# Performance work log

Measured on AMD Instinct MI355X. Metric: run time of the kernel, lower is better.

The kernel has to match this reference:

```python
import jax, jax.numpy as jnp
import numpy as np

NUM_CLUSTERS = 16
CHANNELS = 256
UPDATE_RATE = 0.2
# channels % num_clusters == 0 -> all cluster capacities equal
_BASE = CHANNELS // NUM_CLUSTERS
_REM = CHANNELS % NUM_CLUSTERS
CLUSTER_SIZES = jnp.asarray([_BASE + 1] * _REM + [_BASE] * (NUM_CLUSTERS - _REM), dtype=jnp.int32)


def _cdist(a, b):
    # euclidean pairwise distance, batched over leading dims
    d2 = (jnp.sum(a * a, -1)[..., :, None]
          + jnp.sum(b * b, -1)[..., None, :]
          - 2.0 * (a @ jnp.swapaxes(b, -1, -2)))
    return jnp.sqrt(jnp.clip(d2, 0.0))


def _fps(D, k):
    # farthest point sampling given full [N,N] distance matrix
    start = jnp.argmax(D.sum(1))
    def step(min_d, _):
        far = jnp.argmax(min_d)
        return jnp.minimum(min_d, D[far]), far
    _, rest = jax.lax.scan(step, D[start], None, length=k - 1)
    return jnp.concatenate([start[None], rest])


def _capacity_assign(D, sizes):
    # greedy fixed-capacity assignment, sequential over channels
    order = jnp.argsort(D, axis=1)  # [C, K] cluster preference per channel
    def step(counts, row):
        avail = counts[row] < sizes[row]
        chosen = row[jnp.argmax(avail)]  # first available preference
        return counts.at[chosen].add(1), chosen
    _, assign = jax.lax.scan(step, jnp.zeros(sizes.shape[0], jnp.int32), order)
    return assign


def setup_inputs() -> dict:
    key = jax.random.key(0)
    k1, k2 = jax.random.split(key)
    features = jax.random.normal(k1, (8, CHANNELS, 64, 256), dtype=jnp.float32)
    pos_emb_batch = jax.random.normal(k2, (8, CHANNELS, 3), dtype=jnp.float32)
    return {"features": features, "pos_emb_batch": pos_emb_batch}


def reference(features, pos_emb_batch):
    b, c, nw, df = features.shape
    K = NUM_CLUSTERS
    pos = pos_emb_batch[0]                                   # [C, 3] (module's pos_emb buffer)
    # _initialize_centers: FPS over electrode positions
    centers = pos[_fps(_cdist(pos, pos), K)]                 # [K, 3]
    # _find_farthest_channels (euclidean): FPS over flattened features per batch
    ff = features.reshape(b, c, -1)
    Db = _cdist(ff, ff)                                      # [b, C, C]
    sel = jax.vmap(lambda D: _fps(D, K))(Db)                 # [b, K]
    # _cluster_euclidean_temp: nearest temp center per channel
    center_coords = pos_emb_batch[jnp.arange(b)[:, None], sel]      # [b, K, 3]
    temp_assign = jnp.argmin(_cdist(pos_emb_batch, center_coords), -1)  # [b, C]
    # per-cluster mean of positions over the whole batch
    flat_a = temp_assign.reshape(-1)
    flat_p = pos_emb_batch.reshape(-1, 3)
    sums = jax.ops.segment_sum(flat_p, flat_a, num_segments=K)
    cnts = jax.ops.segment_sum(jnp.ones(flat_a.shape, jnp.float32), flat_a, num_segments=K)
    avg = jnp.where(cnts[:, None] > 0, sums / jnp.maximum(cnts, 1.0)[:, None], 0.0)
    # match old centers to batch-average temp centers and EMA update
    matching = jnp.argmin(_cdist(centers, avg), axis=1)
    centers = (1.0 - UPDATE_RATE) * centers + UPDATE_RATE * avg[matching]
    # capacity-constrained final assignment
    return _capacity_assign(_cdist(pos, centers), CLUSTER_SIZES)
```

## Files before the change

kernel.cpp:

```cpp
#include <hip/hip_runtime.h>

#define NB 8
#define NC 256
#define DF 16384
#define KCL 16
#define SPLITS 16
#define KC (DF / SPLITS)
#define BK 32
#define ITERS (KC / BK)
#define NPAIR 3
#define GEMM_BLOCKS (NPAIR * 2 * NB * SPLITS)

typedef _Float16 half8 __attribute__((ext_vector_type(8)));
typedef _Float16 half4_t __attribute__((ext_vector_type(4)));
typedef float floatx4 __attribute__((ext_vector_type(4)));

__device__ const int TItab[NPAIR] = {0,0,1};
__device__ const int TJtab[NPAIR] = {0,1,1};

__device__ __forceinline__ int argmax256w(float v, float* sv, int* si) {
  int t = threadIdx.x;
  float bv = v; int bi = t;
  #pragma unroll
  for (int s = 32; s >= 1; s >>= 1) {
    float ov = __shfl_down(bv, s);
    int   oi = __shfl_down(bi, s);
    if (ov > bv || (ov == bv && oi < bi)) { bv = ov; bi = oi; }
  }
  int w = t >> 6;
  if ((t & 63) == 0) { sv[w] = bv; si[w] = bi; }
  __syncthreads();
  float rbv = sv[0]; int rbi = si[0];
  #pragma unroll
  for (int k = 1; k < 4; ++k) {
    float ov = sv[k]; int oi = si[k];
    if (ov > rbv || (ov == rbv && oi < rbi)) { rbv = ov; rbi = oi; }
  }
  __syncthreads();
  return rbi;
}

__device__ __forceinline__ int argmax512p(float v, float* sv, int* si) {
  int t = threadIdx.x;
  sv[t] = v; si[t] = t;
  __syncthreads();
  #pragma unroll
  for (int s = 256; s >= 1; s >>= 1) {
    if (t < s) {
      float a = sv[t], b = sv[t + s];
      int ia = si[t], ib = si[t + s];
      if (b > a || (b == a && ib < ia)) { sv[t] = b; si[t] = ib; }
    }
    __syncthreads();
  }
  int r = si[0];
  __syncthreads();
  return r;
}

__global__ __launch_bounds__(512, 6) void k_gemm_pre(const float* __restrict__ ff,
                                                     const float* __restrict__ pe,
                                                     float* __restrict__ Pp,
                                                     float* __restrict__ centers0,
                                                     float* __restrict__ rs,
                                                     float* __restrict__ dgp) {
  __shared__ _Float16 Ah[128][40];
  __shared__ _Float16 Al[128][40];
  __shared__ _Float16 Bh[64][40];
  __shared__ _Float16 Bl[64][40];

  const int bid = blockIdx.x;
  const int tid = threadIdx.x;

  if (bid == GEMM_BLOCKS) {
    float* sm = (float*)&Ah[0][0];
    float* px = sm;        float* py = sm + 256;
    float* pz = sm + 512;  float* pn = sm + 768;
    float* sv = sm + 1024; int*   si = (int*)(sm + 1536);
    int* fpsIdx = (int*)(sm + 2048);
    const int t = tid;
    for (int i = t; i < NB * NC; i += 512) rs[i] = 0.f;
    const bool valid = t < NC;
    float x = 0.f, y = 0.f, z = 0.f, n = 0.f;
    if (valid) {
      x = pe[t * 3 + 0]; y = pe[t * 3 + 1]; z = pe[t * 3 + 2];
      n = x * x + y * y + z * z;
      px[t] = x; py[t] = y; pz[t] = z; pn[t] = n;
    }
    __syncthreads();
    float rsum = -3.4e38f;
    if (valid) {
      rsum = 0.f;
      for (int j = 0; j < NC; ++j) {
        float dot = x * px[j] + y * py[j] + z * pz[j];
        rsum += sqrtf(fmaxf(n + pn[j] - 2.f * dot, 0.f));
      }
    }
    int start = argmax512p(rsum, sv, si);
    if (t == 0) fpsIdx[0] = start;
    float mind = -3.4e38f;
    if (valid) {
      float dot0 = x * px[start] + y * py[start] + z * pz[start];
      mind = sqrtf(fmaxf(n + pn[start] - 2.f * dot0, 0.f));
    }
    for (int it = 1; it < KCL; ++it) {
      int far = argmax512p(mind, sv, si);
      if (t == 0) fpsIdx[it] = far;
      if (valid) {
        float dot = x * px[far] + y * py[far] + z * pz[far];
        mind = fminf(mind, sqrtf(fmaxf(n + pn[far] - 2.f * dot, 0.f)));
      }
    }
    __syncthreads();
    if (t < KCL) {
      int p = fpsIdx[t];
      centers0[t * 3 + 0] = px[p];
      centers0[t * 3 + 1] = py[p];
      centers0[t * 3 + 2] = pz[p];
    }
    return;
  }

  const int x    = bid & 7;
  const int slot = bid >> 3;
  const int tc   = slot % 6;
  const int u    = slot / 6;
  const int gi   = x * 16 + u;
  const int b    = gi & 7;
  const int sp   = gi >> 3;

  const int pair = tc >> 1, ch = tc & 1;
  const int ti = TItab[pair], tj = TJtab[pair];
  const bool diag = (ti == tj);

  const int wave = tid >> 6, lane = tid & 63;
  const int wr = wave >> 1, wc = wave & 1;
  const int lrow = lane & 15, q = lane >> 4;

  const int srA = tid >> 2, scA = (tid & 3) * 8;
  const int srB = tid >> 3, scB = (tid & 7) * 4;
  const float* gA = ff + ((size_t)(b * NC + ti * 128 + srA)) * DF + sp * KC + scA;
  const float* gB = ff + ((size_t)(b * NC + tj * 128 + ch * 64 + srB)) * DF + sp * KC + scB;

  floatx4 a1[2][2], c23[2][2];
  #pragma unroll
  for (int i = 0; i < 2; ++i)
    #pragma unroll
    for (int j = 0; j < 2; ++j) { a1[i][j] = (floatx4)0.f; c23[i][j] = (floatx4)0.f; }

  float4 ra0 = *(const float4*)(gA), ra1 = *(const float4*)(gA + 4);
  float4 rb = make_float4(0.f, 0.f, 0.f, 0.f);
  if (!diag) rb = *(const float4*)(gB);
  gA += BK; gB += BK;

  for (int it = 0; it < ITERS; ++it) {
    float fa[8] = {ra0.x, ra0.y, ra0.z, ra0.w, ra1.x, ra1.y, ra1.z, ra1.w};
    half8 ah, al;
    #pragma unroll
    for (int e = 0; e < 8; ++e) {
      _Float16 h = (_Float16)fa[e];
      ah[e] = h;
      al[e] = (_Float16)(fa[e] - (float)h);
    }
    half4_t bh4 = (half4_t)(_Float16)0.f, bl4 = (half4_t)(_Float16)0.f;
    if (!diag) {
      float fb[4] = {rb.x, rb.y, rb.z, rb.w};
      #pragma unroll
      for (int e = 0; e < 4; ++e) {
        _Float16 h = (_Float16)fb[e];
        bh4[e] = h;
        bl4[e] = (_Float16)(fb[e] - (float)h);
      }
    }
    __syncthreads();
    *(half8*)&Ah[srA][scA] = ah;
    *(half8*)&Al[srA][scA] = al;
    if (!diag) {
      *(half4_t*)&Bh[srB][scB] = bh4;
      *(half4_t*)&Bl[srB][scB] = bl4;
    }
    __syncthreads();
    if (it + 1 < ITERS) {
      ra0 = *(const float4*)(gA); ra1 = *(const float4*)(gA + 4);
      if (!diag) rb = *(const float4*)(gB);
      gA += BK; gB += BK;
    }
    const _Float16* bhp = diag ? &Ah[ch * 64][0] : &Bh[0][0];
    const _Float16* blp = diag ? &Al[ch * 64][0] : &Bl[0][0];
    half8 af[2], lf[2];
    #pragma unroll
    for (int i = 0; i < 2; ++i) {
      af[i] = *(const half8*)&Ah[wr * 32 + i * 16 + lrow][q * 8];
      lf[i] = *(const half8*)&Al[wr * 32 + i * 16 + lrow][q * 8];
    }
    #pragma unroll
    for (int j = 0; j < 2; ++j) {
      half8 bhf = *(const half8*)(bhp + (wc * 32 + j * 16 + lrow) * 40 + q * 8);
      half8 blf = *(const half8*)(blp + (wc * 32 + j * 16 + lrow) * 40 + q * 8);
      #pragma unroll
      for (int i = 0; i < 2; ++i) {
        a1[i][j]  = __builtin_amdgcn_mfma_f32_16x16x32_f16(af[i], bhf, a1[i][j], 0, 0, 0);
        c23[i][j] = __builtin_amdgcn_mfma_f32_16x16x32_f16(af[i], blf, c23[i][j], 0, 0, 0);
        c23[i][j] = __builtin_amdgcn_mfma_f32_16x16x32_f16(lf[i], bhf, c23[i][j], 0, 0, 0);
      }
    }
  }

  float* Pb = Pp + (size_t)(sp * NB + b) * NC * NC;
  #pragma unroll
  for (int i = 0; i < 2; ++i) {
    int grow = ti * 128 + wr * 32 + i * 16 + q * 4;
    #pragma unroll
    for (int j = 0; j < 2; ++j) {
      int gcol = tj * 128 + ch * 64 + wc * 32 + j * 16 + lrow;
      float4 v;
      v.x = a1[i][j][0] + c23[i][j][0];
      v.y = a1[i][j][1] + c23[i][j][1];
      v.z = a1[i][j][2] + c23[i][j][2];
      v.w = a1[i][j][3] + c23[i][j][3];
      Pb[(size_t)(grow + 0) * NC + gcol] = v.x;
      Pb[(size_t)(grow + 1) * NC + gcol] = v.y;
      Pb[(size_t)(grow + 2) * NC + gcol] = v.z;
      Pb[(size_t)(grow + 3) * NC + gcol] = v.w;
      if (!diag) {
        *(float4*)&Pb[(size_t)gcol * NC + grow] = v;
      } else {
        int dr = gcol - grow;
        if (dr >= 0 && dr < 4) {
          float vr = (dr == 0) ? v.x : (dr == 1) ? v.y : (dr == 2) ? v.z : v.w;
          dgp[(sp * NB + b) * NC + gcol] = vr;
        }
      }
    }
  }
}

__global__ __launch_bounds__(256) void k_formD(const float* __restrict__ Pp,
                                               const float* __restrict__ dgp,
                                               float* __restrict__ Db,
                                               float* __restrict__ rs,
                                               int* __restrict__ fps_done) {
  const int t = threadIdx.x;
  const int b = blockIdx.x >> 8;
  const int i = blockIdx.x & 255;
  if (blockIdx.x == 0 && t == 0) *fps_done = 0;
  float dgt = 0.f;
  #pragma unroll
  for (int sp = 0; sp < SPLITS; ++sp)
    dgt += dgp[(sp * NB + b) * NC + t];
  __shared__ float dgi_s;
  if (t == i) dgi_s = dgt;
  __syncthreads();
  float dgi = dgi_s;
  float acc = 0.f;
  #pragma unroll
  for (int sp = 0; sp < SPLITS; ++sp)
    acc += Pp[((size_t)(sp * NB + b) * NC + i) * NC + t];
  float d2 = dgi + dgt - 2.f * acc;
  float d = sqrtf(fmaxf(d2, 0.f));
  Db[((size_t)b * NC + i) * NC + t] = d;
  atomicAdd(&rs[b * NC + t], d);
}

__global__ __launch_bounds__(256) void k_fps_final(const float* __restrict__ Db,
                                                   const float* __restrict__ rs,
                                                   const float* __restrict__ pe,
                                                   const float* __restrict__ centers0,
                                                   float* __restrict__ ccoord,
                                                   int* __restrict__ fps_done,
                                                   int* __restrict__ outp) {
  const int b = blockIdx.x, t = threadIdx.x;
  __shared__ float sv[4]; __shared__ int si[4];
  __shared__ int fpsIdx[KCL];
  {
    const float* D = Db + (size_t)b * NC * NC;
    int start = argmax256w(rs[b * NC + t], sv, si);
    if (t == 0) fpsIdx[0] = start;
    float mind = D[start * NC + t];
    for (int it = 1; it < KCL; ++it) {
      int far = argmax256w(mind, sv, si);
      if (t == 0) fpsIdx[it] = far;
      mind = fminf(mind, D[far * NC + t]);
    }
    __syncthreads();
    if (t < KCL) {
      int p = fpsIdx[t];
      ccoord[(b * KCL + t) * 3 + 0] = pe[(b * NC + p) * 3 + 0];
      ccoord[(b * KCL + t) * 3 + 1] = pe[(b * NC + p) * 3 + 1];
      ccoord[(b * KCL + t) * 3 + 2] = pe[(b * NC + p) * 3 + 2];
    }
  }
  __syncthreads();
  if (t == 0)
    __hip_atomic_fetch_add(fps_done, 1, __ATOMIC_RELEASE, __HIP_MEMORY_SCOPE_AGENT);
  if (b != 0) return;

  if (t == 0) {
    while (__hip_atomic_load(fps_done, __ATOMIC_ACQUIRE, __HIP_MEMORY_SCOPE_AGENT) < NB)
      __builtin_amdgcn_s_sleep(8);
  }
  __syncthreads();

  __shared__ float cc[NB * KCL * 3];
  __shared__ float cn[NB * KCL];
  __shared__ float sums[KCL][3];
  __shared__ int cnts[KCL];
  __shared__ float avg[KCL][3];
  __shared__ float an[KCL];
  __shared__ float c0[KCL * 3];
  __shared__ float c1x[KCL], c1y[KCL], c1z[KCL], c1n[KCL];
  __shared__ int order[NC][KCL];
  for (int i = t; i < NB * KCL * 3; i += 256) cc[i] = ccoord[i];
  if (t < KCL * 3) c0[t] = centers0[t];
  if (t < KCL) { sums[t][0] = 0.f; sums[t][1] = 0.f; sums[t][2] = 0.f; cnts[t] = 0; }
  __syncthreads();
  if (t < NB * KCL) {
    float x = cc[t * 3], y = cc[t * 3 + 1], z = cc[t * 3 + 2];
    cn[t] = x * x + y * y + z * z;
  }
  __syncthreads();
  for (int bb = 0; bb < NB; ++bb) {
    int p = bb * NC + t;
    float x = pe[p * 3], y = pe[p * 3 + 1], z = pe[p * 3 + 2];
    float n = x * x + y * y + z * z;
    float best = 3.4e38f; int bi = 0;
    #pragma unroll
    for (int k = 0; k < KCL; ++k) {
      int c = bb * KCL + k;
      float dot = x * cc[c * 3] + y * cc[c * 3 + 1] + z * cc[c * 3 + 2];
      float d2 = fmaxf(n + cn[c] - 2.f * dot, 0.f);
      if (d2 < best) { best = d2; bi = k; }
    }
    atomicAdd(&sums[bi][0], x);
    atomicAdd(&sums[bi][1], y);
    atomicAdd(&sums[bi][2], z);
    atomicAdd(&cnts[bi], 1);
  }
  __syncthreads();
  if (t < KCL) {
    float c = (float)cnts[t];
    float inv = 1.f / fmaxf(c, 1.f);
    float ax = (cnts[t] > 0) ? sums[t][0] * inv : 0.f;
    float ay = (cnts[t] > 0) ? sums[t][1] * inv : 0.f;
    float az = (cnts[t] > 0) ? sums[t][2] * inv : 0.f;
    avg[t][0] = ax; avg[t][1] = ay; avg[t][2] = az;
    an[t] = ax * ax + ay * ay + az * az;
  }
  __syncthreads();
  if (t < KCL) {
    float x = c0[t * 3], y = c0[t * 3 + 1], z = c0[t * 3 + 2];
    float n = x * x + y * y + z * z;
    float best = 3.4e38f; int bi = 0;
    #pragma unroll
    for (int j = 0; j < KCL; ++j) {
      float dot = x * avg[j][0] + y * avg[j][1] + z * avg[j][2];
      float d2 = fmaxf(n + an[j] - 2.f * dot, 0.f);
      if (d2 < best) { best = d2; bi = j; }
    }
    float nx = 0.8f * x + 0.2f * avg[bi][0];
    float ny = 0.8f * y + 0.2f * avg[bi][1];
    float nz = 0.8f * z + 0.2f * avg[bi][2];
    c1x[t] = nx; c1y[t] = ny; c1z[t] = nz;
    c1n[t] = nx * nx + ny * ny + nz * nz;
  }
  __syncthreads();
  {
    float x = pe[t * 3], y = pe[t * 3 + 1], z = pe[t * 3 + 2];
    float n = x * x + y * y + z * z;
    float v[KCL];
    #pragma unroll
    for (int k = 0; k < KCL; ++k) {
      float dot = x * c1x[k] + y * c1y[k] + z * c1z[k];
      v[k] = fmaxf(n + c1n[k] - 2.f * dot, 0.f);
    }
    bool used[KCL];
    #pragma unroll
    for (int k = 0; k < KCL; ++k) used[k] = false;
    for (int r = 0; r < KCL; ++r) {
      float best = 3.4e38f; int bi = 0;
      #pragma unroll
      for (int j = 0; j < KCL; ++j) {
        if (!used[j] && v[j] < best) { best = v[j]; bi = j; }
      }
      order[t][r] = bi;
      used[bi] = true;
    }
  }
  __syncthreads();
  if (t < 64) {
    int cnt = 0;
    int cur = (t < KCL) ? order[0][t] : 0;
    for (int i = 0; i < NC; ++i) {
      int nxt = (t < KCL && i + 1 < NC) ? order[i + 1][t] : 0;
      int ccur = __shfl(cnt, cur);
      bool avail = (t < KCL) && (ccur < 16);
      unsigned long long m = __ballot(avail);
      int chosen;
      if (m != 0ull) {
        int rank = __ffsll((unsigned long long)m) - 1;
        chosen = __shfl(cur, rank);
      } else {
        chosen = __shfl(cur, 0);
      }
      if (t == chosen) cnt++;
      if (t == 0) outp[i] = chosen;
      cur = nxt;
    }
  }
}

extern "C" void kernel_launch(void* const* d_in, const int* in_sizes, int n_in,
                              void* d_out, int out_size, void* d_ws, size_t ws_size,
                              hipStream_t stream) {
  (void)in_sizes; (void)n_in; (void)out_size; (void)ws_size;
  const float* features = (const float*)d_in[0];
  const float* pe = (const float*)d_in[1];
  char* ws = (char*)d_ws;
  float* Pp       = (float*)(ws);
  float* Db       = (float*)(ws + 33554432);
  float* rs       = (float*)(ws + 35651584);
  float* centers0 = (float*)(ws + 35659776);
  float* ccoord   = (float*)(ws + 35660288);
  float* dgp      = (float*)(ws + 35661824);
  int*   fps_done = (int*)  (ws + 35678208);
  int*   outp     = (int*)d_out;

  hipLaunchKernelGGL(k_gemm_pre, dim3(GEMM_BLOCKS + 1), dim3(512), 0, stream,
                     features, pe, Pp, centers0, rs, dgp);
  hipLaunchKernelGGL(k_formD, dim3(2048), dim3(256), 0, stream,
                     Pp, dgp, Db, rs, fps_done);
  hipLaunchKernelGGL(k_fps_final, dim3(NB), dim3(256), 0, stream,
                     Db, rs, pe, centers0, ccoord, fps_done, outp);
}
```

Before: 339.8 us.

## Double-buffer LDS tiles in split-fp16 Gram GEMM to drop a barrier per iteration

The shared-memory A/B hi/lo tiles become double-buffered, so each iteration converts and stores the next K-slice into the alternate buffer while MFMAs consume the current one. This leaves one __syncthreads per iteration instead of two. The MFMA section is also wrapped in s_setprio raises. LDS use doubles and the occupancy hint drops from 6 to 4 blocks per CU, which could reduce latency hiding for the global loads.

```diff
diff --git a/kernel.cpp b/kernel.cpp
--- a/kernel.cpp
+++ b/kernel.cpp
@@ -58,22 +58,22 @@
   return r;
 }
 
-__global__ __launch_bounds__(512, 6) void k_gemm_pre(const float* __restrict__ ff,
+__global__ __launch_bounds__(512, 4) void k_gemm_pre(const float* __restrict__ ff,
                                                      const float* __restrict__ pe,
                                                      float* __restrict__ Pp,
                                                      float* __restrict__ centers0,
                                                      float* __restrict__ rs,
                                                      float* __restrict__ dgp) {
-  __shared__ _Float16 Ah[128][40];
-  __shared__ _Float16 Al[128][40];
-  __shared__ _Float16 Bh[64][40];
-  __shared__ _Float16 Bl[64][40];
+  __shared__ _Float16 Ah[2][128][40];
+  __shared__ _Float16 Al[2][128][40];
+  __shared__ _Float16 Bh[2][64][40];
+  __shared__ _Float16 Bl[2][64][40];
 
   const int bid = blockIdx.x;
   const int tid = threadIdx.x;
 
   if (bid == GEMM_BLOCKS) {
-    float* sm = (float*)&Ah[0][0];
+    float* sm = (float*)&Ah[0][0][0];
     float* px = sm;        float* py = sm + 256;
     float* pz = sm + 512;  float* pn = sm + 768;
     float* sv = sm + 1024; int*   si = (int*)(sm + 1536);
@@ -152,47 +152,71 @@
   float4 rb = make_float4(0.f, 0.f, 0.f, 0.f);
   if (!diag) rb = *(const float4*)(gB);
   gA += BK; gB += BK;
-
-  for (int it = 0; it < ITERS; ++it) {
+  {
     float fa[8] = {ra0.x, ra0.y, ra0.z, ra0.w, ra1.x, ra1.y, ra1.z, ra1.w};
     half8 ah, al;
     #pragma unroll
     for (int e = 0; e < 8; ++e) {
       _Float16 h = (_Float16)fa[e];
-      ah[e] = h;
-      al[e] = (_Float16)(fa[e] - (float)h);
-    }
-    half4_t bh4 = (half4_t)(_Float16)0.f, bl4 = (half4_t)(_Float16)0.f;
+      ah[e] = h; al[e] = (_Float16)(fa[e] - (float)h);
+    }
+    *(half8*)&Ah[0][srA][scA] = ah;
+    *(half8*)&Al[0][srA][scA] = al;
     if (!diag) {
       float fb[4] = {rb.x, rb.y, rb.z, rb.w};
+      half4_t bh4, bl4;
       #pragma unroll
       for (int e = 0; e < 4; ++e) {
         _Float16 h = (_Float16)fb[e];
-        bh4[e] = h;
-        bl4[e] = (_Float16)(fb[e] - (float)h);
-      }
-    }
-    __syncthreads();
-    *(half8*)&Ah[srA][scA] = ah;
-    *(half8*)&Al[srA][scA] = al;
-    if (!diag) {
-      *(half4_t*)&Bh[srB][scB] = bh4;
-      *(half4_t*)&Bl[srB][scB] = bl4;
-    }
-    __syncthreads();
+        bh4[e] = h; bl4[e] = (_Float16)(fb[e] - (float)h);
+      }
+      *(half4_t*)&Bh[0][srB][scB] = bh4;
+      *(half4_t*)&Bl[0][srB][scB] = bl4;
+    }
+  }
+  ra0 = *(const float4*)(gA); ra1 = *(const float4*)(gA + 4);
+  if (!diag) rb = *(const float4*)(gB);
+  gA += BK; gB += BK;
+  __syncthreads();
+
+  for (int it = 0; it < ITERS; ++it) {
+    const int cur = it & 1;
     if (it + 1 < ITERS) {
-      ra0 = *(const float4*)(gA); ra1 = *(const float4*)(gA + 4);
-      if (!diag) rb = *(const float4*)(gB);
-      gA += BK; gB += BK;
-    }
-    const _Float16* bhp = diag ? &Ah[ch * 64][0] : &Bh[0][0];
-    const _Float16* blp = diag ? &Al[ch * 64][0] : &Bl[0][0];
+      float fa[8] = {ra0.x, ra0.y, ra0.z, ra0.w, ra1.x, ra1.y, ra1.z, ra1.w};
+      half8 ah, al;
+      #pragma unroll
+      for (int e = 0; e < 8; ++e) {
+        _Float16 h = (_Float16)fa[e];
+        ah[e] = h; al[e] = (_Float16)(fa[e] - (float)h);
+      }
+      *(half8*)&Ah[cur ^ 1][srA][scA] = ah;
+      *(half8*)&Al[cur ^ 1][srA][scA] = al;
+      if (!diag) {
+        float fb[4] = {rb.x, rb.y, rb.z, rb.w};
+        half4_t bh4, bl4;
+        #pragma unroll
+        for (int e = 0; e < 4; ++e) {
+          _Float16 h = (_Float16)fb[e];
+          bh4[e] = h; bl4[e] = (_Float16)(fb[e] - (float)h);
+        }
+        *(half4_t*)&Bh[cur ^ 1][srB][scB] = bh4;
+        *(half4_t*)&Bl[cur ^ 1][srB][scB] = bl4;
+      }
+      if (it + 2 < ITERS) {
+        ra0 = *(const float4*)(gA); ra1 = *(const float4*)(gA + 4);
+        if (!diag) rb = *(const float4*)(gB);
+        gA += BK; gB += BK;
+      }
+    }
+    const _Float16* bhp = diag ? &Ah[cur][ch * 64][0] : &Bh[cur][0][0];
+    const _Float16* blp = diag ? &Al[cur][ch * 64][0] : &Bl[cur][0][0];
     half8 af[2], lf[2];
     #pragma unroll
     for (int i = 0; i < 2; ++i) {
-      af[i] = *(const half8*)&Ah[wr * 32 + i * 16 + lrow][q * 8];
-      lf[i] = *(const half8*)&Al[wr * 32 + i * 16 + lrow][q * 8];
-    }
+      af[i] = *(const half8*)&Ah[cur][wr * 32 + i * 16 + lrow][q * 8];
+      lf[i] = *(const half8*)&Al[cur][wr * 32 + i * 16 + lrow][q * 8];
+    }
+    __builtin_amdgcn_s_setprio(1);
     #pragma unroll
     for (int j = 0; j < 2; ++j) {
       half8 bhf = *(const half8*)(bhp + (wc * 32 + j * 16 + lrow) * 40 + q * 8);
@@ -204,6 +228,8 @@
         c23[i][j] = __builtin_amdgcn_mfma_f32_16x16x32_f16(lf[i], bhf, c23[i][j], 0, 0, 0);
       }
     }
+    __builtin_amdgcn_s_setprio(0);
+    __syncthreads();
   }
 
   float* Pb = Pp + (size_t)(sp * NB + b) * NC * NC;
```

After: 329.0 us (median of 2 runs). 3.2% less time.
